# Kernel tuning notes

Hardware: AMD Instinct MI355X
Metric: run time of the kernel (lower is better)

The kernel has to match this reference:

```python
import jax, jax.numpy as jnp
import numpy as np

N = 40962      # icosahedral mesh nodes
E = 245760     # ~degree-6 mesh edges
HD = 256       # hidden_dim
H = 8          # heads
C = HD // H    # out_ch per head = 32
EDIM = 16      # raw edge feature dim
L = 4          # num_layers


def setup_inputs() -> dict:
    key = jax.random.key(0)
    ks = iter(jax.random.split(key, 48))
    def rn(shape, scale=0.05):
        return jax.random.normal(next(ks), shape, dtype=jnp.float32) * scale
    inp = {}
    inp['mesh_enc'] = jax.random.normal(next(ks), (N, HD), dtype=jnp.float32)
    inp['edge_index'] = jax.random.randint(next(ks), (2, E), 0, N)
    inp['edge_attr'] = jax.random.normal(next(ks), (E, EDIM), dtype=jnp.float32)
    # edge input projection
    inp['ep_W'] = rn((EDIM, HD)); inp['ep_b'] = jnp.zeros((HD,), jnp.float32)
    # GATv2 layer 0 (in_ch=HD) and layers 1..L-1 stacked (in_ch=C)
    inp['Wl0'] = rn((HD, H, C));  inp['Wr0'] = rn((HD, H, C))
    inp['Wl'] = rn((L - 1, C, H, C)); inp['Wr'] = rn((L - 1, C, H, C))
    inp['We0'] = rn((HD, H, C));  inp['We'] = rn((L - 1, HD, H, C))
    inp['att0'] = rn((H, C));     inp['att'] = rn((L - 1, H, C))
    inp['Wres0'] = rn((HD, C));   inp['Wres'] = rn((L - 1, C, C))
    inp['bn0'] = jnp.zeros((C,), jnp.float32); inp['bn'] = jnp.zeros((L - 1, C), jnp.float32)
    # edge-update MLP (upd_hidden_dim = hidden_dim * ffn_ratio = HD)
    inp['Wu1_0'] = rn((2 * C + HD, HD)); inp['Wu1'] = rn((L - 1, 2 * C + HD, HD))
    inp['bu1_0'] = jnp.zeros((HD,), jnp.float32); inp['bu1'] = jnp.zeros((L - 1, HD), jnp.float32)
    inp['Wu2_0'] = rn((HD, HD)); inp['Wu2'] = rn((L - 1, HD, HD))
    inp['bu2_0'] = jnp.zeros((HD,), jnp.float32); inp['bu2'] = jnp.zeros((L - 1, HD), jnp.float32)
    # inter-layer LayerNorms (L-1 of them, over C)
    inp['ln_g'] = jnp.ones((L - 1, C), jnp.float32); inp['ln_b'] = jnp.zeros((L - 1, C), jnp.float32)
    # SGFormer-style global branch
    inp['Wq'] = rn((HD, H, C)); inp['Wk'] = rn((HD, H, C)); inp['Wv'] = rn((HD, H, C))
    inp['alpha_p'] = jnp.array(0.5, jnp.float32)
    inp['cn_g'] = jnp.ones((C,), jnp.float32); inp['cn_b'] = jnp.zeros((C,), jnp.float32)
    return inp


def _layernorm(x, g, b):
    mu = x.mean(-1, keepdims=True)
    var = x.var(-1, keepdims=True)
    return (x - mu) / jnp.sqrt(var + 1e-5) * g + b


def _segment_softmax(s, dst, n):
    smax = jax.ops.segment_max(s, dst, num_segments=n)
    smax = jnp.where(jnp.isfinite(smax), smax, 0.0)
    ex = jnp.exp(s - smax[dst])
    den = jax.ops.segment_sum(ex, dst, num_segments=n)
    return ex / (den[dst] + 1e-16)


def _gat(x, e, src, dst, Wl, Wr, We, att, Wres, bn, Wu1, bu1, Wu2, bu2):
    # GATv2 with edge features (PyG semantics), concat=False (head mean), residual
    xl = jnp.einsum('nd,dhc->nhc', x, Wl)          # [N,H,C]
    xr = jnp.einsum('nd,dhc->nhc', x, Wr)
    ee = jnp.einsum('ed,dhc->ehc', e, We)          # [E,H,C]
    m = xl[src] + xr[dst] + ee
    s = jnp.einsum('ehc,hc->eh', jax.nn.leaky_relu(m, 0.2), att)
    a = _segment_softmax(s, dst, x.shape[0])       # [E,H]
    agg = jax.ops.segment_sum(a[:, :, None] * xl[src], dst, num_segments=x.shape[0])
    out = agg.mean(axis=1) + x @ Wres + bn         # [N,C]
    # residual edge update MLP
    h = jnp.concatenate([out[src], out[dst], e], axis=-1)
    e_new = e + jax.nn.gelu(h @ Wu1 + bu1) @ Wu2 + bu2
    return out, e_new


def _sgformer(x, Wq, Wk, Wv):
    # SGFormer linear global attention, O(N)
    q = jnp.einsum('nd,dhc->nhc', x, Wq)
    k = jnp.einsum('nd,dhc->nhc', x, Wk)
    v = jnp.einsum('nd,dhc->nhc', x, Wv)
    qs = q / (jnp.linalg.norm(q, axis=-1, keepdims=True) + 1e-6)
    ks = k / (jnp.linalg.norm(k, axis=-1, keepdims=True) + 1e-6)
    n = jnp.float32(x.shape[0])
    kv = jnp.einsum('nhc,nhd->hcd', ks, v)
    num = jnp.einsum('nhc,hcd->nhd', qs, kv) + n * v
    den = jnp.einsum('nhc,hc->nh', qs, ks.sum(0)) + n
    return (num / den[..., None]).mean(axis=1)     # [N,C]


def reference(mesh_enc, edge_index, edge_attr, ep_W, ep_b, Wl0, Wr0, Wl, Wr, We0, We,
              att0, att, Wres0, Wres, bn0, bn, Wu1_0, Wu1, bu1_0, bu1, Wu2_0, Wu2,
              bu2_0, bu2, ln_g, ln_b, Wq, Wk, Wv, alpha_p, cn_g, cn_b):
    src, dst = edge_index[0], edge_index[1]
    e = edge_attr @ ep_W + ep_b
    x, e = _gat(mesh_enc, e, src, dst, Wl0, Wr0, We0, att0, Wres0, bn0,
                Wu1_0, bu1_0, Wu2_0, bu2_0)
    x = _layernorm(x, ln_g[0], ln_b[0])
    for i in range(L - 1):
        x, e = _gat(x, e, src, dst, Wl[i], Wr[i], We[i], att[i], Wres[i], bn[i],
                    Wu1[i], bu1[i], Wu2[i], bu2[i])
        if i < L - 2:
            x = _layernorm(x, ln_g[i + 1], ln_b[i + 1])
    trans_out = _sgformer(mesh_enc, Wq, Wk, Wv)
    alpha = jax.nn.sigmoid(alpha_p)
    return _layernorm(alpha * x + (1.0 - alpha) * trans_out, cn_g, cn_b)
```

## Files before the change

### kernel.cpp

```cpp
#include <hip/hip_runtime.h>
#include <hip/hip_bf16.h>
#include <math.h>

typedef __hip_bfloat16 bf16;
typedef __attribute__((ext_vector_type(8))) __bf16 bf16x8;
typedef __attribute__((ext_vector_type(4))) float f32x4;

#define NN 40962
#define NE 245760
#define HDIM 256
#define NH 8
#define CH 32

#define MT 64
#define KVB 512

__device__ __forceinline__ float b2f(bf16 v) { return __bfloat162float(v); }
__device__ __forceinline__ bf16 f2b(float v) { return __float2bfloat16(v); }
__device__ __forceinline__ unsigned short f2bs(float v) {
  bf16 b = __float2bfloat16(v);
  return __builtin_bit_cast(unsigned short, b);
}
__device__ __forceinline__ float bs2f(unsigned short u) {
  return __bfloat162float(__builtin_bit_cast(bf16, u));
}

__device__ __forceinline__ float fast_gelu(float x) {
  float x2 = x * x;
  float g = x * (0.7978845608028654f + 0.0356774081f * x2);
  float y = fminf(g * 2.885390081777927f, 60.f);
  float t = exp2f(y);
  float th = (t - 1.f) * __builtin_amdgcn_rcpf(t + 1.f);
  return 0.5f * x * (1.f + th);
}

__global__ void k_edge_proj(const float* __restrict__ attr, const float* __restrict__ W,
                            const float* __restrict__ b, bf16* __restrict__ e) {
  int t = blockIdx.x * 256 + threadIdx.x;
  int ed = t >> 5;
  int q  = t & 31;
  int j0 = q * 8;
  float acc[8];
#pragma unroll
  for (int i = 0; i < 8; ++i) acc[i] = b[j0 + i];
  float ar[16];
#pragma unroll
  for (int k = 0; k < 16; ++k) ar[k] = attr[ed * 16 + k];
#pragma unroll
  for (int k = 0; k < 16; ++k) {
    float4 w0 = *reinterpret_cast<const float4*>(&W[k * HDIM + j0]);
    float4 w1 = *reinterpret_cast<const float4*>(&W[k * HDIM + j0 + 4]);
    acc[0] += ar[k] * w0.x; acc[1] += ar[k] * w0.y;
    acc[2] += ar[k] * w0.z; acc[3] += ar[k] * w0.w;
    acc[4] += ar[k] * w1.x; acc[5] += ar[k] * w1.y;
    acc[6] += ar[k] * w1.z; acc[7] += ar[k] * w1.w;
  }
  unsigned short ov[8];
#pragma unroll
  for (int i = 0; i < 8; ++i) ov[i] = f2bs(acc[i]);
  *reinterpret_cast<uint4*>(&e[(size_t)ed * HDIM + j0]) =
      *reinterpret_cast<const uint4*>(ov);
}

__global__ void k_zero_i(int* __restrict__ p, int n) {
  int i = blockIdx.x * blockDim.x + threadIdx.x;
  if (i < n) p[i] = 0;
}
__global__ void k_copy_i(const int* __restrict__ a, int* __restrict__ b, int n) {
  int i = blockIdx.x * blockDim.x + threadIdx.x;
  if (i < n) b[i] = a[i];
}

__global__ void k_csr_count(const int* __restrict__ dst, int* __restrict__ cnt) {
  int e = blockIdx.x * 256 + threadIdx.x;
  if (e < NE) atomicAdd(&cnt[dst[e]], 1);
}
__global__ void k_csr_scan(const int* __restrict__ cnt, int* __restrict__ rowptr) {
  __shared__ int part[256];
  __shared__ int tot;
  int t = threadIdx.x;
  const int CHUNK = (NN + 255) / 256;
  int lo = t * CHUNK, hi = lo + CHUNK; if (hi > NN) hi = NN; if (lo > NN) lo = NN;
  int s = 0;
  for (int i = lo; i < hi; ++i) s += cnt[i];
  part[t] = s;
  __syncthreads();
  if (t == 0) {
    int run = 0;
    for (int i = 0; i < 256; ++i) { int v = part[i]; part[i] = run; run += v; }
    tot = run;
  }
  __syncthreads();
  int run = part[t];
  for (int i = lo; i < hi; ++i) { rowptr[i] = run; run += cnt[i]; }
  if (t == 0) rowptr[NN] = tot;
}
__global__ void k_csr_fill(const int* __restrict__ src, const int* __restrict__ dst,
                           int* __restrict__ cursor, int2* __restrict__ csr) {
  int e = blockIdx.x * 256 + threadIdx.x;
  if (e >= NE) return;
  int p = atomicAdd(&cursor[dst[e]], 1);
  int2 v; v.x = e; v.y = src[e];
  csr[p] = v;
}

template <int K>
__global__ void k_swz_w(const float* __restrict__ W, unsigned short* __restrict__ out) {
  int t = blockIdx.x * 256 + threadIdx.x;
  if (t >= K * 256) return;
  int i  = t & 7;
  int l  = (t >> 3) & 63;
  int k0 = (t >> 9) % (K / 32);
  int n0 = t / (512 * (K / 32));
  int k = k0 * 32 + (l >> 4) * 8 + i;
  int n = n0 * 16 + (l & 15);
  out[t] = f2bs(W[k * 256 + n]);
}

__global__ void k_swz_all(const float* __restrict__ We0, const float* __restrict__ WeL,
                          const float* __restrict__ Wl0, const float* __restrict__ Wr0,
                          const float* __restrict__ Wq, const float* __restrict__ Wk,
                          const float* __restrict__ Wv, unsigned short* __restrict__ dst) {
  int mat = blockIdx.x >> 8;
  int t = ((blockIdx.x & 255) << 8) | threadIdx.x;
  const float* W;
  switch (mat) {
    case 0: W = We0; break;
    case 1: W = WeL; break;
    case 2: W = WeL + 65536; break;
    case 3: W = WeL + 131072; break;
    case 4: W = Wl0; break;
    case 5: W = Wr0; break;
    case 6: W = Wq; break;
    case 7: W = Wk; break;
    default: W = Wv; break;
  }
  int i  = t & 7;
  int l  = (t >> 3) & 63;
  int k0 = (t >> 9) & 7;
  int n0 = t >> 12;
  int k = k0 * 32 + (l >> 4) * 8 + i;
  int n = n0 * 16 + (l & 15);
  dst[(size_t)mat * 65536 + t] = f2bs(W[k * 256 + n]);
}

__global__ __launch_bounds__(512) void k_edge_score_mfma(
    const bf16* __restrict__ e, const unsigned short* __restrict__ Wes,
    const bf16* __restrict__ xl, const bf16* __restrict__ xr,
    const float* __restrict__ att, const int* __restrict__ src,
    const int* __restrict__ dst, float* __restrict__ sx) {
  __shared__ unsigned short Ae[MT][264];
  __shared__ unsigned short Xs[MT][264];
  __shared__ float attS[HDIM];
  __shared__ int sidx[MT], didx[MT];
  int tid = threadIdx.x, l = tid & 63, w = tid >> 6;
  int lr = l & 15, lk = l >> 4;
  int base = blockIdx.x * MT;
  if (tid < HDIM) attS[tid] = att[tid];
  if (tid < MT) sidx[tid] = src[base + tid];
  else if (tid < 2 * MT) didx[tid - MT] = dst[base + tid - MT];
  __syncthreads();
  for (int t = tid; t < MT * 32; t += 512) {
    int p = t >> 5, c = t & 31;
    *reinterpret_cast<uint4*>(&Ae[p][c * 8]) =
        *reinterpret_cast<const uint4*>(&e[(size_t)(base + p) * HDIM + c * 8]);
  }
  for (int t = tid; t < MT * 32; t += 512) {
    int p = t >> 5, c = t & 31;
    uint4 ul = *reinterpret_cast<const uint4*>(&xl[(size_t)sidx[p] * HDIM + c * 8]);
    uint4 ur = *reinterpret_cast<const uint4*>(&xr[(size_t)didx[p] * HDIM + c * 8]);
    const unsigned short* al = (const unsigned short*)&ul;
    const unsigned short* ar = (const unsigned short*)&ur;
    unsigned short ov[8];
#pragma unroll
    for (int i = 0; i < 8; ++i) ov[i] = f2bs(bs2f(al[i]) + bs2f(ar[i]));
    *reinterpret_cast<uint4*>(&Xs[p][c * 8]) = *reinterpret_cast<const uint4*>(ov);
  }
  __syncthreads();

  int j0 = w * 32;
  f32x4 acc[4][2];
#pragma unroll
  for (int m = 0; m < 4; ++m)
#pragma unroll
    for (int n = 0; n < 2; ++n)
#pragma unroll
      for (int r = 0; r < 4; ++r) acc[m][n][r] = 0.f;
  for (int k0 = 0; k0 < 8; ++k0) {
    bf16x8 a[4], b[2];
#pragma unroll
    for (int m = 0; m < 4; ++m)
      a[m] = *reinterpret_cast<const bf16x8*>(&Ae[m * 16 + lr][k0 * 32 + lk * 8]);
#pragma unroll
    for (int n = 0; n < 2; ++n) {
      int nt = w * 2 + n;
      b[n] = *reinterpret_cast<const bf16x8*>(Wes + ((size_t)(nt * 8 + k0) * 64 + l) * 8);
    }
#pragma unroll
    for (int m = 0; m < 4; ++m)
#pragma unroll
      for (int n = 0; n < 2; ++n)
        acc[m][n] = __builtin_amdgcn_mfma_f32_16x16x32_bf16(a[m], b[n], acc[m][n], 0, 0, 0);
  }
#pragma unroll
  for (int n = 0; n < 2; ++n) {
    int col = j0 + n * 16 + lr;
    float av = attS[col];
#pragma unroll
    for (int m = 0; m < 4; ++m)
#pragma unroll
      for (int r = 0; r < 4; ++r) {
        int row = m * 16 + lk * 4 + r;
        float mm = acc[m][n][r] + bs2f(Xs[row][col]);
        mm = (mm > 0.f) ? mm : 0.2f * mm;
        Xs[row][col] = f2bs(mm * av);
      }
  }
  __syncthreads();
  for (int pair = tid; pair < MT * NH; pair += 512) {
    int ed = pair >> 3, h = pair & 7;
    float s = 0.f;
#pragma unroll
    for (int c = 0; c < CH; ++c) s += bs2f(Xs[ed][h * CH + c]);
    sx[(size_t)(base + ed) * NH + h] = expf(s);
  }
}

template <int ID, bool LN>
__global__ __launch_bounds__(256) void k_gat_out(
    const int* __restrict__ rowptr, const int2* __restrict__ csr,
    const float* __restrict__ sx, const bf16* __restrict__ xl,
    const float* __restrict__ x, const float* __restrict__ Wres,
    const float* __restrict__ bn, const float* __restrict__ lng,
    const float* __restrict__ lnb, float* __restrict__ xpre,
    float* __restrict__ xpost) {
  int n = blockIdx.x;
  int j = threadIdx.x;
  int h = j >> 5, c = j & 31;
  int p0 = rowptr[n], p1 = rowptr[n + 1];
  float a = 0.f, dsum = 0.f;
  for (int p = p0; p < p1; ++p) {
    int2 es = csr[p];
    float ex = sx[(size_t)es.x * NH + h];
    a += ex * b2f(xl[(size_t)es.y * HDIM + j]);
    dsum += ex;
  }
  __shared__ float oh[HDIM];
  __shared__ float rs[NH][CH];
  __shared__ float oc[CH + 1];
  oh[j] = a / (dsum + 1e-16f);
  const int KS = ID / NH;
  float r = 0.f;
  for (int k = h * KS; k < (h + 1) * KS; ++k)
    r += x[(size_t)n * ID + k] * Wres[k * CH + c];
  rs[h][c] = r;
  __syncthreads();
  if (j < CH) {
    float o = 0.f;
#pragma unroll
    for (int hh = 0; hh < NH; ++hh) o += oh[hh * CH + j];
    o *= (1.f / NH);
    float rr = 0.f;
#pragma unroll
    for (int hh = 0; hh < NH; ++hh) rr += rs[hh][j];
    o += rr + bn[j];
    xpre[(size_t)n * CH + j] = o;
    oc[j] = o;
  }
  __syncthreads();
  if (LN && j < CH) {
    float mu = 0.f;
#pragma unroll
    for (int k = 0; k < CH; ++k) mu += oc[k];
    mu *= (1.f / CH);
    float var = 0.f;
#pragma unroll
    for (int k = 0; k < CH; ++k) { float d = oc[k] - mu; var += d * d; }
    var *= (1.f / CH);
    xpost[(size_t)n * CH + j] = (oc[j] - mu) * rsqrtf(var + 1e-5f) * lng[j] + lnb[j];
  }
}

__global__ __launch_bounds__(512) void k_edge_mlp_mfma(
    bf16* __restrict__ e, const float* __restrict__ xo,
    const int* __restrict__ src, const int* __restrict__ dst,
    const unsigned short* __restrict__ W1s, const float* __restrict__ bu1,
    const unsigned short* __restrict__ W2s, const float* __restrict__ bu2) {
  __shared__ unsigned short A1s[MT][328];
  __shared__ unsigned short A2s[MT][264];
  __shared__ int sidx[MT], didx[MT];
  int tid = threadIdx.x;
  int l = tid & 63;
  int w = tid >> 6;
  int base = blockIdx.x * MT;
  int lr = l & 15;
  int lk = l >> 4;

  if (tid < MT) sidx[tid] = src[base + tid];
  else if (tid < 2 * MT) didx[tid - MT] = dst[base + tid - MT];
  __syncthreads();

  for (int t = tid; t < MT * 32; t += 512) {
    int p = t >> 5, cc = t & 31;
    uint4 v = *reinterpret_cast<const uint4*>(&e[(size_t)(base + p) * HDIM + cc * 8]);
    *reinterpret_cast<uint4*>(&A1s[p][64 + cc * 8]) = v;
  }
  for (int t = tid; t < MT * 64; t += 512) {
    int p = t >> 6, c = t & 63;
    float v = (c < CH) ? xo[(size_t)sidx[p] * CH + c]
                       : xo[(size_t)didx[p] * CH + (c - CH)];
    A1s[p][c] = f2bs(v);
  }
  __syncthreads();

  int j0 = w * 32;

  f32x4 acc[4][2];
#pragma unroll
  for (int m = 0; m < 4; ++m)
#pragma unroll
    for (int n = 0; n < 2; ++n)
#pragma unroll
      for (int r = 0; r < 4; ++r) acc[m][n][r] = 0.f;

  for (int k0 = 0; k0 < 10; ++k0) {
    bf16x8 a[4], b[2];
#pragma unroll
    for (int m = 0; m < 4; ++m)
      a[m] = *reinterpret_cast<const bf16x8*>(&A1s[m * 16 + lr][k0 * 32 + lk * 8]);
#pragma unroll
    for (int n = 0; n < 2; ++n) {
      int nt = w * 2 + n;
      b[n] = *reinterpret_cast<const bf16x8*>(W1s + ((size_t)(nt * 10 + k0) * 64 + l) * 8);
    }
#pragma unroll
    for (int m = 0; m < 4; ++m)
#pragma unroll
      for (int n = 0; n < 2; ++n)
        acc[m][n] = __builtin_amdgcn_mfma_f32_16x16x32_bf16(a[m], b[n], acc[m][n], 0, 0, 0);
  }

#pragma unroll
  for (int n = 0; n < 2; ++n) {
    float bv = bu1[j0 + n * 16 + lr];
#pragma unroll
    for (int m = 0; m < 4; ++m)
#pragma unroll
      for (int r = 0; r < 4; ++r) {
        float g = fast_gelu(acc[m][n][r] + bv);
        A2s[m * 16 + lk * 4 + r][j0 + n * 16 + lr] = f2bs(g);
      }
  }
  __syncthreads();

#pragma unroll
  for (int m = 0; m < 4; ++m)
#pragma unroll
    for (int n = 0; n < 2; ++n)
#pragma unroll
      for (int r = 0; r < 4; ++r) acc[m][n][r] = 0.f;

  for (int k0 = 0; k0 < 8; ++k0) {
    bf16x8 a[4], b[2];
#pragma unroll
    for (int m = 0; m < 4; ++m)
      a[m] = *reinterpret_cast<const bf16x8*>(&A2s[m * 16 + lr][k0 * 32 + lk * 8]);
#pragma unroll
    for (int n = 0; n < 2; ++n) {
      int nt = w * 2 + n;
      b[n] = *reinterpret_cast<const bf16x8*>(W2s + ((size_t)(nt * 8 + k0) * 64 + l) * 8);
    }
#pragma unroll
    for (int m = 0; m < 4; ++m)
#pragma unroll
      for (int n = 0; n < 2; ++n)
        acc[m][n] = __builtin_amdgcn_mfma_f32_16x16x32_bf16(a[m], b[n], acc[m][n], 0, 0, 0);
  }
  __syncthreads();

#pragma unroll
  for (int n = 0; n < 2; ++n) {
    int col = j0 + n * 16 + lr;
    float bv = bu2[col];
#pragma unroll
    for (int m = 0; m < 4; ++m)
#pragma unroll
      for (int r = 0; r < 4; ++r) {
        int row = m * 16 + lk * 4 + r;
        float eo = bs2f(A1s[row][64 + col]);
        A2s[row][col] = f2bs(eo + acc[m][n][r] + bv);
      }
  }
  __syncthreads();

  for (int t = tid; t < MT * 32; t += 512) {
    int p = t >> 5, cc = t & 31;
    *reinterpret_cast<uint4*>(&e[(size_t)(base + p) * HDIM + cc * 8]) =
        *reinterpret_cast<const uint4*>(&A2s[p][cc * 8]);
  }
}

__global__ __launch_bounds__(256) void k_node_proj0_mfma(
    const float* __restrict__ x, const unsigned short* __restrict__ Wls,
    const unsigned short* __restrict__ Wrs, bf16* __restrict__ xl,
    bf16* __restrict__ xr) {
  __shared__ unsigned short A[MT][264];
  __shared__ unsigned short O[MT][264];
  int tid = threadIdx.x, l = tid & 63, w = tid >> 6;
  int lr = l & 15, lk = l >> 4;
  int base = blockIdx.x * MT;
  for (int t = tid; t < MT * 64; t += 256) {
    int p = t >> 6, c = t & 63;
    int row = base + p; if (row >= NN) row = NN - 1;
    float4 v = *reinterpret_cast<const float4*>(&x[(size_t)row * HDIM + c * 4]);
    unsigned short tmp[4] = {f2bs(v.x), f2bs(v.y), f2bs(v.z), f2bs(v.w)};
    *reinterpret_cast<uint2*>(&A[p][c * 4]) = *reinterpret_cast<const uint2*>(tmp);
  }
  __syncthreads();
  int j0 = w * 64;
#pragma unroll
  for (int mtx = 0; mtx < 2; ++mtx) {
    const unsigned short* Ws = (mtx == 0) ? Wls : Wrs;
    bf16* outp = (mtx == 0) ? xl : xr;
    f32x4 acc[4][4];
#pragma unroll
    for (int m = 0; m < 4; ++m)
#pragma unroll
      for (int n = 0; n < 4; ++n)
#pragma unroll
        for (int r = 0; r < 4; ++r) acc[m][n][r] = 0.f;
    for (int k0 = 0; k0 < 8; ++k0) {
      bf16x8 a[4], b[4];
#pragma unroll
      for (int m = 0; m < 4; ++m)
        a[m] = *reinterpret_cast<const bf16x8*>(&A[m * 16 + lr][k0 * 32 + lk * 8]);
#pragma unroll
      for (int n = 0; n < 4; ++n) {
        int nt = (j0 >> 4) + n;
        b[n] = *reinterpret_cast<const bf16x8*>(Ws + ((size_t)(nt * 8 + k0) * 64 + l) * 8);
      }
#pragma unroll
      for (int m = 0; m < 4; ++m)
#pragma unroll
        for (int n = 0; n < 4; ++n)
          acc[m][n] = __builtin_amdgcn_mfma_f32_16x16x32_bf16(a[m], b[n], acc[m][n], 0, 0, 0);
    }
#pragma unroll
    for (int n = 0; n < 4; ++n)
#pragma unroll
      for (int m = 0; m < 4; ++m)
#pragma unroll
        for (int r = 0; r < 4; ++r)
          O[m * 16 + lk * 4 + r][j0 + n * 16 + lr] = f2bs(acc[m][n][r]);
    __syncthreads();
    for (int t = tid; t < MT * 32; t += 256) {
      int p = t >> 5, c = t & 31;
      if (base + p < NN)
        *reinterpret_cast<uint4*>(&outp[(size_t)(base + p) * HDIM + c * 8]) =
            *reinterpret_cast<const uint4*>(&O[p][c * 8]);
    }
    __syncthreads();
  }
}

__global__ __launch_bounds__(256) void k_node_projS_mfma(
    const float* __restrict__ x, const unsigned short* __restrict__ Wls,
    const unsigned short* __restrict__ Wrs, bf16* __restrict__ xl,
    bf16* __restrict__ xr) {
  __shared__ unsigned short A[MT][40];
  __shared__ unsigned short O[MT][264];
  int tid = threadIdx.x, l = tid & 63, w = tid >> 6;
  int lr = l & 15, lk = l >> 4;
  int base = blockIdx.x * MT;
  for (int t = tid; t < MT * 8; t += 256) {
    int p = t >> 3, q = t & 7;
    int row = base + p; if (row >= NN) row = NN - 1;
    float4 v = *reinterpret_cast<const float4*>(&x[(size_t)row * CH + q * 4]);
    unsigned short tmp[4] = {f2bs(v.x), f2bs(v.y), f2bs(v.z), f2bs(v.w)};
    *reinterpret_cast<uint2*>(&A[p][q * 4]) = *reinterpret_cast<const uint2*>(tmp);
  }
  __syncthreads();
  int j0 = w * 64;
#pragma unroll
  for (int mtx = 0; mtx < 2; ++mtx) {
    const unsigned short* Ws = (mtx == 0) ? Wls : Wrs;
    bf16* outp = (mtx == 0) ? xl : xr;
    f32x4 acc[4][4];
#pragma unroll
    for (int m = 0; m < 4; ++m)
#pragma unroll
      for (int n = 0; n < 4; ++n)
#pragma unroll
        for (int r = 0; r < 4; ++r) acc[m][n][r] = 0.f;
    bf16x8 a[4], b[4];
#pragma unroll
    for (int m = 0; m < 4; ++m)
      a[m] = *reinterpret_cast<const bf16x8*>(&A[m * 16 + lr][lk * 8]);
#pragma unroll
    for (int n = 0; n < 4; ++n) {
      int nt = (j0 >> 4) + n;
      b[n] = *reinterpret_cast<const bf16x8*>(Ws + ((size_t)nt * 64 + l) * 8);
    }
#pragma unroll
    for (int m = 0; m < 4; ++m)
#pragma unroll
      for (int n = 0; n < 4; ++n)
        acc[m][n] = __builtin_amdgcn_mfma_f32_16x16x32_bf16(a[m], b[n], acc[m][n], 0, 0, 0);
#pragma unroll
    for (int n = 0; n < 4; ++n)
#pragma unroll
      for (int m = 0; m < 4; ++m)
#pragma unroll
        for (int r = 0; r < 4; ++r)
          O[m * 16 + lk * 4 + r][j0 + n * 16 + lr] = f2bs(acc[m][n][r]);
    __syncthreads();
    for (int t = tid; t < MT * 32; t += 256) {
      int p = t >> 5, c = t & 31;
      if (base + p < NN)
        *reinterpret_cast<uint4*>(&outp[(size_t)(base + p) * HDIM + c * 8]) =
            *reinterpret_cast<const uint4*>(&O[p][c * 8]);
    }
    __syncthreads();
  }
}

__global__ __launch_bounds__(256) void k_sg_qkv_mfma(
    const float* __restrict__ x, const unsigned short* __restrict__ Wqs,
    const unsigned short* __restrict__ Wks, const unsigned short* __restrict__ Wvs,
    bf16* __restrict__ qs, bf16* __restrict__ ks, bf16* __restrict__ vv) {
  __shared__ unsigned short A[MT][264];
  __shared__ unsigned short O[MT][264];
  int tid = threadIdx.x, l = tid & 63, w = tid >> 6;
  int lr = l & 15, lk = l >> 4;
  int base = blockIdx.x * MT;
  for (int t = tid; t < MT * 64; t += 256) {
    int p = t >> 6, c = t & 63;
    int row = base + p; if (row >= NN) row = NN - 1;
    float4 v = *reinterpret_cast<const float4*>(&x[(size_t)row * HDIM + c * 4]);
    unsigned short tmp[4] = {f2bs(v.x), f2bs(v.y), f2bs(v.z), f2bs(v.w)};
    *reinterpret_cast<uint2*>(&A[p][c * 4]) = *reinterpret_cast<const uint2*>(tmp);
  }
  __syncthreads();
  int j0 = w * 64;
#pragma unroll
  for (int mtx = 0; mtx < 3; ++mtx) {
    const unsigned short* Ws = (mtx == 0) ? Wqs : (mtx == 1) ? Wks : Wvs;
    bf16* outp = (mtx == 0) ? qs : (mtx == 1) ? ks : vv;
    f32x4 acc[4][4];
#pragma unroll
    for (int m = 0; m < 4; ++m)
#pragma unroll
      for (int n = 0; n < 4; ++n)
#pragma unroll
        for (int r = 0; r < 4; ++r) acc[m][n][r] = 0.f;
    for (int k0 = 0; k0 < 8; ++k0) {
      bf16x8 a[4], b[4];
#pragma unroll
      for (int m = 0; m < 4; ++m)
        a[m] = *reinterpret_cast<const bf16x8*>(&A[m * 16 + lr][k0 * 32 + lk * 8]);
#pragma unroll
      for (int n = 0; n < 4; ++n) {
        int nt = (j0 >> 4) + n;
        b[n] = *reinterpret_cast<const bf16x8*>(Ws + ((size_t)(nt * 8 + k0) * 64 + l) * 8);
      }
#pragma unroll
      for (int m = 0; m < 4; ++m)
#pragma unroll
        for (int n = 0; n < 4; ++n)
          acc[m][n] = __builtin_amdgcn_mfma_f32_16x16x32_bf16(a[m], b[n], acc[m][n], 0, 0, 0);
    }
    if (mtx < 2) {
      float pa[4][4], pb[4][4];
#pragma unroll
      for (int m = 0; m < 4; ++m)
#pragma unroll
        for (int r = 0; r < 4; ++r) {
          pa[m][r] = acc[m][0][r] * acc[m][0][r] + acc[m][1][r] * acc[m][1][r];
          pb[m][r] = acc[m][2][r] * acc[m][2][r] + acc[m][3][r] * acc[m][3][r];
        }
#pragma unroll
      for (int off = 1; off < 16; off <<= 1) {
#pragma unroll
        for (int m = 0; m < 4; ++m)
#pragma unroll
          for (int r = 0; r < 4; ++r) {
            pa[m][r] += __shfl_xor(pa[m][r], off);
            pb[m][r] += __shfl_xor(pb[m][r], off);
          }
      }
#pragma unroll
      for (int m = 0; m < 4; ++m)
#pragma unroll
        for (int r = 0; r < 4; ++r) {
          float ra = 1.f / (sqrtf(pa[m][r]) + 1e-6f);
          float rb = 1.f / (sqrtf(pb[m][r]) + 1e-6f);
          acc[m][0][r] *= ra; acc[m][1][r] *= ra;
          acc[m][2][r] *= rb; acc[m][3][r] *= rb;
        }
    }
#pragma unroll
    for (int n = 0; n < 4; ++n)
#pragma unroll
      for (int m = 0; m < 4; ++m)
#pragma unroll
        for (int r = 0; r < 4; ++r)
          O[m * 16 + lk * 4 + r][j0 + n * 16 + lr] = f2bs(acc[m][n][r]);
    __syncthreads();
    for (int t = tid; t < MT * 32; t += 256) {
      int p = t >> 5, c = t & 31;
      if (base + p < NN)
        *reinterpret_cast<uint4*>(&outp[(size_t)(base + p) * HDIM + c * 8]) =
            *reinterpret_cast<const uint4*>(&O[p][c * 8]);
    }
    __syncthreads();
  }
}

__global__ void k_sg_kv1(const bf16* __restrict__ ks, const bf16* __restrict__ vv,
                         float* __restrict__ part) {
  int t = threadIdx.x;
  int h = t >> 5;
  float kvloc[CH];
  float ksl = 0.f;
#pragma unroll
  for (int d = 0; d < CH; ++d) kvloc[d] = 0.f;
  __shared__ float krow[HDIM], vrow[HDIM];
  for (int n = blockIdx.x; n < NN; n += KVB) {
    krow[t] = b2f(ks[(size_t)n * HDIM + t]);
    vrow[t] = b2f(vv[(size_t)n * HDIM + t]);
    __syncthreads();
    float kc = krow[t];
    ksl += kc;
#pragma unroll
    for (int d = 0; d < CH; ++d) kvloc[d] += kc * vrow[h * CH + d];
    __syncthreads();
  }
  float* dstp = part + (size_t)blockIdx.x * 8448;
#pragma unroll
  for (int d = 0; d < CH; d += 4)
    *reinterpret_cast<float4*>(&dstp[t * CH + d]) =
        *reinterpret_cast<const float4*>(&kvloc[d]);
  dstp[8192 + t] = ksl;
}

__global__ void k_sg_kv2(const float* __restrict__ part, float* __restrict__ kv,
                         float* __restrict__ ksum) {
  int idx = blockIdx.x * 256 + threadIdx.x;
  if (idx >= 8448) return;
  float s = 0.f;
  for (int b = 0; b < KVB; ++b) s += part[(size_t)b * 8448 + idx];
  if (idx < 8192) kv[idx] = s;
  else ksum[idx - 8192] = s;
}

__global__ void k_sg_final(const bf16* __restrict__ qs, const bf16* __restrict__ vv,
                           const float* __restrict__ kv, const float* __restrict__ ksum,
                           const float* __restrict__ xg, const float* __restrict__ alphap,
                           const float* __restrict__ cng, const float* __restrict__ cnb,
                           float* __restrict__ out) {
  int t = threadIdx.x;
  int d = t & 31, sub = t >> 5;
  __shared__ float qrow[8][HDIM];
  __shared__ float crow[8][CH];
  int n = blockIdx.x * 8 + sub;
  for (int tt = t; tt < 8 * HDIM; tt += 256) {
    int p = tt >> 8, k = tt & 255;
    int n2 = blockIdx.x * 8 + p;
    if (n2 < NN) qrow[p][k] = b2f(qs[(size_t)n2 * HDIM + k]);
  }
  __syncthreads();
  float alpha = 1.f / (1.f + expf(-alphap[0]));
  const float Nf = (float)NN;
  float comb = 0.f;
  if (n < NN) {
    float acc = 0.f;
#pragma unroll
    for (int h = 0; h < NH; ++h) {
      float nm = 0.f, dp = 0.f;
#pragma unroll 8
      for (int c = 0; c < CH; ++c) {
        float qv = qrow[sub][h * CH + c];
        nm += qv * kv[(h * CH + c) * CH + d];
        dp += qv * ksum[h * CH + c];
      }
      nm += Nf * b2f(vv[(size_t)n * HDIM + h * CH + d]);
      acc += nm / (dp + Nf);
    }
    float trans = acc * (1.f / NH);
    comb = alpha * xg[(size_t)n * CH + d] + (1.f - alpha) * trans;
    crow[sub][d] = comb;
  }
  __syncthreads();
  if (n < NN) {
    float mu = 0.f;
#pragma unroll
    for (int k = 0; k < CH; ++k) mu += crow[sub][k];
    mu *= (1.f / CH);
    float var = 0.f;
#pragma unroll
    for (int k = 0; k < CH; ++k) { float dv = crow[sub][k] - mu; var += dv * dv; }
    var *= (1.f / CH);
    float o = (comb - mu) * rsqrtf(var + 1e-5f) * cng[d] + cnb[d];
    out[(size_t)n * CH + d] = o;
  }
}

extern "C" void kernel_launch(void* const* d_in, const int* in_sizes, int n_in,
                              void* d_out, int out_size, void* d_ws, size_t ws_size,
                              hipStream_t stream) {
  const float* mesh  = (const float*)d_in[0];
  const int*   eidx  = (const int*)d_in[1];
  const float* eattr = (const float*)d_in[2];
  const float* epW   = (const float*)d_in[3];
  const float* epb   = (const float*)d_in[4];
  const float* Wl0   = (const float*)d_in[5];
  const float* Wr0   = (const float*)d_in[6];
  const float* WlL   = (const float*)d_in[7];
  const float* WrL   = (const float*)d_in[8];
  const float* We0   = (const float*)d_in[9];
  const float* WeL   = (const float*)d_in[10];
  const float* att0  = (const float*)d_in[11];
  const float* attL  = (const float*)d_in[12];
  const float* Wres0 = (const float*)d_in[13];
  const float* WresL = (const float*)d_in[14];
  const float* bn0   = (const float*)d_in[15];
  const float* bnL   = (const float*)d_in[16];
  const float* Wu1_0 = (const float*)d_in[17];
  const float* Wu1L  = (const float*)d_in[18];
  const float* bu1_0 = (const float*)d_in[19];
  const float* bu1L  = (const float*)d_in[20];
  const float* Wu2_0 = (const float*)d_in[21];
  const float* Wu2L  = (const float*)d_in[22];
  const float* bu2_0 = (const float*)d_in[23];
  const float* bu2L  = (const float*)d_in[24];
  const float* lng   = (const float*)d_in[25];
  const float* lnb   = (const float*)d_in[26];
  const float* Wq    = (const float*)d_in[27];
  const float* Wk    = (const float*)d_in[28];
  const float* Wv    = (const float*)d_in[29];
  const float* alphap= (const float*)d_in[30];
  const float* cng   = (const float*)d_in[31];
  const float* cnb   = (const float*)d_in[32];

  const int* src = eidx;
  const int* dst = eidx + NE;

  char* base = (char*)d_ws;
  size_t o = 0;
  auto alloc = [&](size_t bytes) -> char* {
    o = (o + 255) & ~(size_t)255;
    char* p = base + o;
    o += bytes;
    return p;
  };
  bf16* e    = (bf16*)alloc((size_t)NE * HDIM * 2);
  bf16* xl   = (bf16*)alloc((size_t)NN * HDIM * 2);
  bf16* xr   = (bf16*)alloc((size_t)NN * HDIM * 2);
  bf16* vvb  = (bf16*)alloc((size_t)NN * HDIM * 2);
  float* sbuf= (float*)alloc((size_t)NE * NH * 4);
  float* xa  = (float*)alloc((size_t)NN * CH * 4);
  float* xb  = (float*)alloc((size_t)NN * CH * 4);
  float* xc  = (float*)alloc((size_t)NN * CH * 4);
  float* kv  = (float*)alloc(NH * CH * CH * 4);
  float* ksum= (float*)alloc(NH * CH * 4);
  float* kvpart = (float*)alloc((size_t)KVB * 8448 * 4);
  unsigned short* w1s = (unsigned short*)alloc((size_t)3 * 320 * 256 * 2);
  unsigned short* w2s = (unsigned short*)alloc((size_t)3 * 256 * 256 * 2);
  unsigned short* wall= (unsigned short*)alloc((size_t)9 * 65536 * 2);
  unsigned short* w32s= (unsigned short*)alloc((size_t)6 * 32 * 256 * 2);
  int* cnt    = (int*)alloc((size_t)NN * 4);
  int* rowptr = (int*)alloc((size_t)(NN + 1) * 4);
  int* cursor = (int*)alloc((size_t)NN * 4);
  int2* csr   = (int2*)alloc((size_t)NE * 8);
  if (ws_size < o) return;

  for (int i = 0; i < 3; ++i) {
    const float* W1 = (i == 0) ? Wu1_0 : Wu1L + (size_t)(i - 1) * 320 * 256;
    const float* W2 = (i == 0) ? Wu2_0 : Wu2L + (size_t)(i - 1) * 256 * 256;
    k_swz_w<320><<<320, 256, 0, stream>>>(W1, w1s + (size_t)i * 320 * 256);
    k_swz_w<256><<<256, 256, 0, stream>>>(W2, w2s + (size_t)i * 256 * 256);
  }
  k_swz_all<<<9 * 256, 256, 0, stream>>>(We0, WeL, Wl0, Wr0, Wq, Wk, Wv, wall);
  for (int i = 0; i < 3; ++i) {
    k_swz_w<32><<<32, 256, 0, stream>>>(WlL + (size_t)i * 32 * 256,
                                        w32s + (size_t)(i * 2 + 0) * 8192);
    k_swz_w<32><<<32, 256, 0, stream>>>(WrL + (size_t)i * 32 * 256,
                                        w32s + (size_t)(i * 2 + 1) * 8192);
  }

  k_zero_i<<<(NN + 255) / 256, 256, 0, stream>>>(cnt, NN);
  k_csr_count<<<(NE + 255) / 256, 256, 0, stream>>>(dst, cnt);
  k_csr_scan<<<1, 256, 0, stream>>>(cnt, rowptr);
  k_copy_i<<<(NN + 255) / 256, 256, 0, stream>>>(rowptr, cursor, NN);
  k_csr_fill<<<(NE + 255) / 256, 256, 0, stream>>>(src, dst, cursor, csr);

  k_edge_proj<<<NE * 32 / 256, 256, 0, stream>>>(eattr, epW, epb, e);

  const float* xin = mesh;
  float* post = xb;
  for (int l = 0; l < 4; ++l) {
    const float *att_p, *Wres_p, *bn_p, *bu1_p, *bu2_p;
    if (l == 0) {
      att_p = att0; Wres_p = Wres0; bn_p = bn0; bu1_p = bu1_0; bu2_p = bu2_0;
    } else {
      int i = l - 1;
      att_p = attL + (size_t)i * HDIM;
      Wres_p = WresL + (size_t)i * CH * CH;
      bn_p = bnL + (size_t)i * CH;
      bu1_p = bu1L + (size_t)i * HDIM;
      bu2_p = bu2L + (size_t)i * HDIM;
    }

    if (l == 0)
      k_node_proj0_mfma<<<(NN + MT - 1) / MT, 256, 0, stream>>>(
          mesh, wall + (size_t)4 * 65536, wall + (size_t)5 * 65536, xl, xr);
    else
      k_node_projS_mfma<<<(NN + MT - 1) / MT, 256, 0, stream>>>(
          xin, w32s + (size_t)((l - 1) * 2 + 0) * 8192,
          w32s + (size_t)((l - 1) * 2 + 1) * 8192, xl, xr);

    k_edge_score_mfma<<<NE / MT, 512, 0, stream>>>(e, wall + (size_t)l * 65536,
                                                   xl, xr, att_p, src, dst, sbuf);

    if (l == 0)
      k_gat_out<HDIM, true><<<NN, 256, 0, stream>>>(rowptr, csr, sbuf, xl, xin, Wres_p,
                                                    bn_p, lng, lnb, xa, post);
    else if (l < 3)
      k_gat_out<CH, true><<<NN, 256, 0, stream>>>(rowptr, csr, sbuf, xl, xin, Wres_p,
                                                  bn_p, lng + (size_t)l * CH,
                                                  lnb + (size_t)l * CH, xa, post);
    else
      k_gat_out<CH, false><<<NN, 256, 0, stream>>>(rowptr, csr, sbuf, xl, xin, Wres_p,
                                                   bn_p, nullptr, nullptr, xa, nullptr);

    if (l < 3)
      k_edge_mlp_mfma<<<NE / MT, 512, 0, stream>>>(e, xa, src, dst,
                                                   w1s + (size_t)l * 320 * 256, bu1_p,
                                                   w2s + (size_t)l * 256 * 256, bu2_p);

    xin = post;
    post = (post == xb) ? xc : xb;
  }

  k_sg_qkv_mfma<<<(NN + MT - 1) / MT, 256, 0, stream>>>(
      mesh, wall + (size_t)6 * 65536, wall + (size_t)7 * 65536,
      wall + (size_t)8 * 65536, xl, xr, vvb);
  k_sg_kv1<<<KVB, 256, 0, stream>>>(xr, vvb, kvpart);
  k_sg_kv2<<<33, 256, 0, stream>>>(kvpart, kv, ksum);
  k_sg_final<<<(NN + 7) / 8, 256, 0, stream>>>(xl, vvb, kv, ksum, xa, alphap, cng, cnb,
                                               (float*)d_out);
}
```

Measured before the change: 1.689 ms.

## Fuse setup kernels and cut LDS footprint in edge score and edge MLP

All weight-swizzle launches and the count-zeroing kernel become one launch, and the cursor copy is folded into the CSR scan, removing about fifteen small launches. The edge-score kernel drops its second LDS tile and reads xl/xr directly in the epilogue, reusing the Ae buffer. The edge-update MLP shares one LDS buffer for both stages and adds the residual by rereading e from global memory. Smaller LDS use should raise occupancy, at the cost of uncoalesced 2-byte gathers in the score epilogue and an extra global read of e.

```diff
diff --git a/kernel.cpp b/kernel.cpp
--- a/kernel.cpp
+++ b/kernel.cpp
@@ -62,20 +62,12 @@
       *reinterpret_cast<const uint4*>(ov);
 }
 
-__global__ void k_zero_i(int* __restrict__ p, int n) {
-  int i = blockIdx.x * blockDim.x + threadIdx.x;
-  if (i < n) p[i] = 0;
-}
-__global__ void k_copy_i(const int* __restrict__ a, int* __restrict__ b, int n) {
-  int i = blockIdx.x * blockDim.x + threadIdx.x;
-  if (i < n) b[i] = a[i];
-}
-
 __global__ void k_csr_count(const int* __restrict__ dst, int* __restrict__ cnt) {
   int e = blockIdx.x * 256 + threadIdx.x;
   if (e < NE) atomicAdd(&cnt[dst[e]], 1);
 }
-__global__ void k_csr_scan(const int* __restrict__ cnt, int* __restrict__ rowptr) {
+__global__ void k_csr_scan(const int* __restrict__ cnt, int* __restrict__ rowptr,
+                           int* __restrict__ cursor) {
   __shared__ int part[256];
   __shared__ int tot;
   int t = threadIdx.x;
@@ -92,7 +84,7 @@
   }
   __syncthreads();
   int run = part[t];
-  for (int i = lo; i < hi; ++i) { rowptr[i] = run; run += cnt[i]; }
+  for (int i = lo; i < hi; ++i) { rowptr[i] = run; cursor[i] = run; run += cnt[i]; }
   if (t == 0) rowptr[NN] = tot;
 }
 __global__ void k_csr_fill(const int* __restrict__ src, const int* __restrict__ dst,
@@ -104,44 +96,62 @@
   csr[p] = v;
 }
 
-template <int K>
-__global__ void k_swz_w(const float* __restrict__ W, unsigned short* __restrict__ out) {
-  int t = blockIdx.x * 256 + threadIdx.x;
-  if (t >= K * 256) return;
-  int i  = t & 7;
-  int l  = (t >> 3) & 63;
-  int k0 = (t >> 9) % (K / 32);
-  int n0 = t / (512 * (K / 32));
+struct SwzP {
+  const float *We0, *WeL, *Wl0, *Wr0, *Wq, *Wk, *Wv;
+  const float *Wu1_0, *Wu1L, *Wu2_0, *Wu2L, *WlL, *WrL;
+  unsigned short *wall, *w1s, *w2s, *w32s;
+  int* cnt;
+};
+__device__ __forceinline__ void swz1(const float* __restrict__ W,
+                                     unsigned short* __restrict__ out, int t, int Kdiv32) {
+  int i = t & 7, l = (t >> 3) & 63;
+  int k0 = (t >> 9) % Kdiv32;
+  int n0 = t / (512 * Kdiv32);
   int k = k0 * 32 + (l >> 4) * 8 + i;
   int n = n0 * 16 + (l & 15);
   out[t] = f2bs(W[k * 256 + n]);
 }
-
-__global__ void k_swz_all(const float* __restrict__ We0, const float* __restrict__ WeL,
-                          const float* __restrict__ Wl0, const float* __restrict__ Wr0,
-                          const float* __restrict__ Wq, const float* __restrict__ Wk,
-                          const float* __restrict__ Wv, unsigned short* __restrict__ dst) {
-  int mat = blockIdx.x >> 8;
-  int t = ((blockIdx.x & 255) << 8) | threadIdx.x;
-  const float* W;
-  switch (mat) {
-    case 0: W = We0; break;
-    case 1: W = WeL; break;
-    case 2: W = WeL + 65536; break;
-    case 3: W = WeL + 131072; break;
-    case 4: W = Wl0; break;
-    case 5: W = Wr0; break;
-    case 6: W = Wq; break;
-    case 7: W = Wk; break;
-    default: W = Wv; break;
-  }
-  int i  = t & 7;
-  int l  = (t >> 3) & 63;
-  int k0 = (t >> 9) & 7;
-  int n0 = t >> 12;
-  int k = k0 * 32 + (l >> 4) * 8 + i;
-  int n = n0 * 16 + (l & 15);
-  dst[(size_t)mat * 65536 + t] = f2bs(W[k * 256 + n]);
+#define SWZ_NW (9 * 65536)
+#define SWZ_N1 (3 * 81920)
+#define SWZ_N2 (3 * 65536)
+#define SWZ_N3 (6 * 8192)
+__global__ void k_swz_fused(SwzP P) {
+  int gid = blockIdx.x * 256 + threadIdx.x;
+  if (gid < SWZ_NW) {
+    int mat = gid >> 16, t = gid & 65535;
+    const float* W;
+    switch (mat) {
+      case 0: W = P.We0; break;
+      case 1: W = P.WeL; break;
+      case 2: W = P.WeL + 65536; break;
+      case 3: W = P.WeL + 131072; break;
+      case 4: W = P.Wl0; break;
+      case 5: W = P.Wr0; break;
+      case 6: W = P.Wq; break;
+      case 7: W = P.Wk; break;
+      default: W = P.Wv; break;
+    }
+    swz1(W, P.wall + (size_t)mat * 65536, t, 8);
+  } else if (gid < SWZ_NW + SWZ_N1) {
+    int idx = gid - SWZ_NW;
+    int mat = idx / 81920, t = idx % 81920;
+    const float* W = (mat == 0) ? P.Wu1_0 : P.Wu1L + (size_t)(mat - 1) * 81920;
+    swz1(W, P.w1s + (size_t)mat * 81920, t, 10);
+  } else if (gid < SWZ_NW + SWZ_N1 + SWZ_N2) {
+    int idx = gid - SWZ_NW - SWZ_N1;
+    int mat = idx >> 16, t = idx & 65535;
+    const float* W = (mat == 0) ? P.Wu2_0 : P.Wu2L + (size_t)(mat - 1) * 65536;
+    swz1(W, P.w2s + (size_t)mat * 65536, t, 8);
+  } else if (gid < SWZ_NW + SWZ_N1 + SWZ_N2 + SWZ_N3) {
+    int idx = gid - SWZ_NW - SWZ_N1 - SWZ_N2;
+    int mat = idx >> 13, t = idx & 8191;
+    int i = mat >> 1;
+    const float* W = (mat & 1) ? P.WrL + (size_t)i * 8192 : P.WlL + (size_t)i * 8192;
+    swz1(W, P.w32s + (size_t)mat * 8192, t, 1);
+  } else {
+    int i = gid - (SWZ_NW + SWZ_N1 + SWZ_N2 + SWZ_N3);
+    if (i < NN) P.cnt[i] = 0;
+  }
 }
 
 __global__ __launch_bounds__(512) void k_edge_score_mfma(
@@ -150,7 +160,6 @@
     const float* __restrict__ att, const int* __restrict__ src,
     const int* __restrict__ dst, float* __restrict__ sx) {
   __shared__ unsigned short Ae[MT][264];
-  __shared__ unsigned short Xs[MT][264];
   __shared__ float attS[HDIM];
   __shared__ int sidx[MT], didx[MT];
   int tid = threadIdx.x, l = tid & 63, w = tid >> 6;
@@ -159,26 +168,13 @@
   if (tid < HDIM) attS[tid] = att[tid];
   if (tid < MT) sidx[tid] = src[base + tid];
   else if (tid < 2 * MT) didx[tid - MT] = dst[base + tid - MT];
-  __syncthreads();
   for (int t = tid; t < MT * 32; t += 512) {
     int p = t >> 5, c = t & 31;
     *reinterpret_cast<uint4*>(&Ae[p][c * 8]) =
         *reinterpret_cast<const uint4*>(&e[(size_t)(base + p) * HDIM + c * 8]);
   }
-  for (int t = tid; t < MT * 32; t += 512) {
-    int p = t >> 5, c = t & 31;
-    uint4 ul = *reinterpret_cast<const uint4*>(&xl[(size_t)sidx[p] * HDIM + c * 8]);
-    uint4 ur = *reinterpret_cast<const uint4*>(&xr[(size_t)didx[p] * HDIM + c * 8]);
-    const unsigned short* al = (const unsigned short*)&ul;
-    const unsigned short* ar = (const unsigned short*)&ur;
-    unsigned short ov[8];
-#pragma unroll
-    for (int i = 0; i < 8; ++i) ov[i] = f2bs(bs2f(al[i]) + bs2f(ar[i]));
-    *reinterpret_cast<uint4*>(&Xs[p][c * 8]) = *reinterpret_cast<const uint4*>(ov);
-  }
-  __syncthreads();
-
-  int j0 = w * 32;
+  __syncthreads();
+
   f32x4 acc[4][2];
 #pragma unroll
   for (int m = 0; m < 4; ++m)
@@ -202,18 +198,22 @@
       for (int n = 0; n < 2; ++n)
         acc[m][n] = __builtin_amdgcn_mfma_f32_16x16x32_bf16(a[m], b[n], acc[m][n], 0, 0, 0);
   }
+  __syncthreads();
+
 #pragma unroll
   for (int n = 0; n < 2; ++n) {
-    int col = j0 + n * 16 + lr;
+    int col = w * 32 + n * 16 + lr;
     float av = attS[col];
 #pragma unroll
     for (int m = 0; m < 4; ++m)
 #pragma unroll
       for (int r = 0; r < 4; ++r) {
         int row = m * 16 + lk * 4 + r;
-        float mm = acc[m][n][r] + bs2f(Xs[row][col]);
+        float xs = b2f(xl[(size_t)sidx[row] * HDIM + col]) +
+                   b2f(xr[(size_t)didx[row] * HDIM + col]);
+        float mm = acc[m][n][r] + xs;
         mm = (mm > 0.f) ? mm : 0.2f * mm;
-        Xs[row][col] = f2bs(mm * av);
+        Ae[row][col] = f2bs(mm * av);
       }
   }
   __syncthreads();
@@ -221,7 +221,7 @@
     int ed = pair >> 3, h = pair & 7;
     float s = 0.f;
 #pragma unroll
-    for (int c = 0; c < CH; ++c) s += bs2f(Xs[ed][h * CH + c]);
+    for (int c = 0; c < CH; ++c) s += bs2f(Ae[ed][h * CH + c]);
     sx[(size_t)(base + ed) * NH + h] = expf(s);
   }
 }
@@ -286,8 +286,7 @@
     const int* __restrict__ src, const int* __restrict__ dst,
     const unsigned short* __restrict__ W1s, const float* __restrict__ bu1,
     const unsigned short* __restrict__ W2s, const float* __restrict__ bu2) {
-  __shared__ unsigned short A1s[MT][328];
-  __shared__ unsigned short A2s[MT][264];
+  __shared__ unsigned short buf[MT][328];
   __shared__ int sidx[MT], didx[MT];
   int tid = threadIdx.x;
   int l = tid & 63;
@@ -303,13 +302,13 @@
   for (int t = tid; t < MT * 32; t += 512) {
     int p = t >> 5, cc = t & 31;
     uint4 v = *reinterpret_cast<const uint4*>(&e[(size_t)(base + p) * HDIM + cc * 8]);
-    *reinterpret_cast<uint4*>(&A1s[p][64 + cc * 8]) = v;
+    *reinterpret_cast<uint4*>(&buf[p][64 + cc * 8]) = v;
   }
   for (int t = tid; t < MT * 64; t += 512) {
     int p = t >> 6, c = t & 63;
     float v = (c < CH) ? xo[(size_t)sidx[p] * CH + c]
                        : xo[(size_t)didx[p] * CH + (c - CH)];
-    A1s[p][c] = f2bs(v);
+    buf[p][c] = f2bs(v);
   }
   __syncthreads();
 
@@ -327,7 +326,7 @@
     bf16x8 a[4], b[2];
 #pragma unroll
     for (int m = 0; m < 4; ++m)
-      a[m] = *reinterpret_cast<const bf16x8*>(&A1s[m * 16 + lr][k0 * 32 + lk * 8]);
+      a[m] = *reinterpret_cast<const bf16x8*>(&buf[m * 16 + lr][k0 * 32 + lk * 8]);
 #pragma unroll
     for (int n = 0; n < 2; ++n) {
       int nt = w * 2 + n;
@@ -339,6 +338,7 @@
       for (int n = 0; n < 2; ++n)
         acc[m][n] = __builtin_amdgcn_mfma_f32_16x16x32_bf16(a[m], b[n], acc[m][n], 0, 0, 0);
   }
+  __syncthreads();
 
 #pragma unroll
   for (int n = 0; n < 2; ++n) {
@@ -348,7 +348,7 @@
 #pragma unroll
       for (int r = 0; r < 4; ++r) {
         float g = fast_gelu(acc[m][n][r] + bv);
-        A2s[m * 16 + lk * 4 + r][j0 + n * 16 + lr] = f2bs(g);
+        buf[m * 16 + lk * 4 + r][j0 + n * 16 + lr] = f2bs(g);
       }
   }
   __syncthreads();
@@ -364,7 +364,7 @@
     bf16x8 a[4], b[2];
 #pragma unroll
     for (int m = 0; m < 4; ++m)
-      a[m] = *reinterpret_cast<const bf16x8*>(&A2s[m * 16 + lr][k0 * 32 + lk * 8]);
+      a[m] = *reinterpret_cast<const bf16x8*>(&buf[m * 16 + lr][k0 * 32 + lk * 8]);
 #pragma unroll
     for (int n = 0; n < 2; ++n) {
       int nt = w * 2 + n;
@@ -385,18 +385,22 @@
 #pragma unroll
     for (int m = 0; m < 4; ++m)
 #pragma unroll
-      for (int r = 0; r < 4; ++r) {
-        int row = m * 16 + lk * 4 + r;
-        float eo = bs2f(A1s[row][64 + col]);
-        A2s[row][col] = f2bs(eo + acc[m][n][r] + bv);
-      }
+      for (int r = 0; r < 4; ++r)
+        buf[m * 16 + lk * 4 + r][col] = f2bs(acc[m][n][r] + bv);
   }
   __syncthreads();
 
   for (int t = tid; t < MT * 32; t += 512) {
     int p = t >> 5, cc = t & 31;
+    uint4 dv = *reinterpret_cast<const uint4*>(&buf[p][cc * 8]);
+    uint4 ev = *reinterpret_cast<const uint4*>(&e[(size_t)(base + p) * HDIM + cc * 8]);
+    const unsigned short* dd = (const unsigned short*)&dv;
+    const unsigned short* ee = (const unsigned short*)&ev;
+    unsigned short ov[8];
+#pragma unroll
+    for (int i = 0; i < 8; ++i) ov[i] = f2bs(bs2f(ee[i]) + bs2f(dd[i]));
     *reinterpret_cast<uint4*>(&e[(size_t)(base + p) * HDIM + cc * 8]) =
-        *reinterpret_cast<const uint4*>(&A2s[p][cc * 8]);
+        *reinterpret_cast<const uint4*>(ov);
   }
 }
 
@@ -774,24 +778,16 @@
   int2* csr   = (int2*)alloc((size_t)NE * 8);
   if (ws_size < o) return;
 
-  for (int i = 0; i < 3; ++i) {
-    const float* W1 = (i == 0) ? Wu1_0 : Wu1L + (size_t)(i - 1) * 320 * 256;
-    const float* W2 = (i == 0) ? Wu2_0 : Wu2L + (size_t)(i - 1) * 256 * 256;
-    k_swz_w<320><<<320, 256, 0, stream>>>(W1, w1s + (size_t)i * 320 * 256);
-    k_swz_w<256><<<256, 256, 0, stream>>>(W2, w2s + (size_t)i * 256 * 256);
-  }
-  k_swz_all<<<9 * 256, 256, 0, stream>>>(We0, WeL, Wl0, Wr0, Wq, Wk, Wv, wall);
-  for (int i = 0; i < 3; ++i) {
-    k_swz_w<32><<<32, 256, 0, stream>>>(WlL + (size_t)i * 32 * 256,
-                                        w32s + (size_t)(i * 2 + 0) * 8192);
-    k_swz_w<32><<<32, 256, 0, stream>>>(WrL + (size_t)i * 32 * 256,
-                                        w32s + (size_t)(i * 2 + 1) * 8192);
-  }
-
-  k_zero_i<<<(NN + 255) / 256, 256, 0, stream>>>(cnt, NN);
+  SwzP P;
+  P.We0 = We0; P.WeL = WeL; P.Wl0 = Wl0; P.Wr0 = Wr0; P.Wq = Wq; P.Wk = Wk; P.Wv = Wv;
+  P.Wu1_0 = Wu1_0; P.Wu1L = Wu1L; P.Wu2_0 = Wu2_0; P.Wu2L = Wu2L;
+  P.WlL = WlL; P.WrL = WrL;
+  P.wall = wall; P.w1s = w1s; P.w2s = w2s; P.w32s = w32s; P.cnt = cnt;
+  int swz_total = SWZ_NW + SWZ_N1 + SWZ_N2 + SWZ_N3 + NN;
+  k_swz_fused<<<(swz_total + 255) / 256, 256, 0, stream>>>(P);
+
   k_csr_count<<<(NE + 255) / 256, 256, 0, stream>>>(dst, cnt);
-  k_csr_scan<<<1, 256, 0, stream>>>(cnt, rowptr);
-  k_copy_i<<<(NN + 255) / 256, 256, 0, stream>>>(rowptr, cursor, NN);
+  k_csr_scan<<<1, 256, 0, stream>>>(cnt, rowptr, cursor);
   k_csr_fill<<<(NE + 255) / 256, 256, 0, stream>>>(src, dst, cursor, csr);
 
   k_edge_proj<<<NE * 32 / 256, 256, 0, stream>>>(eattr, epW, epb, e);
```

New measurement: 1.601 ms. 1.06x faster.
